# Performance work log

Measured on AMD Instinct MI355X. Metric: run time of the kernel, lower is better.

Reference implementation:

```python
import jax, jax.numpy as jnp
import numpy as np

B, T, N, F_IN, F_OUT = 2, 8, 8192, 128, 32

def setup_inputs() -> dict:
    key = jax.random.key(0)
    k1, k2, k3, k4 = jax.random.split(key, 4)
    inp = jax.random.normal(k1, (B, T, N, F_IN), dtype=jnp.float32)
    adj = jax.random.randint(k2, (N, N), 0, 2, dtype=jnp.int32)
    # xavier_uniform with gain=1.414 ~ std = gain*sqrt(2/(fan_in+fan_out)); gaussian approx
    w_std = 1.414 * np.sqrt(2.0 / (F_IN + F_OUT))
    a_std = 1.414 * np.sqrt(2.0 / (2 * F_OUT + N))
    W = jax.random.normal(k3, (F_IN, F_OUT), dtype=jnp.float32) * w_std
    a = jax.random.normal(k4, (2 * F_OUT, N), dtype=jnp.float32) * a_std
    return {"inp": inp, "adj": adj, "W": W, "a": a}

def reference(inp, adj, W, a):
    # h: [B,T,N,out]
    h = jnp.einsum('btni,io->btno', inp, W)
    out = W.shape[1]
    # mask[j,i] = 1 if j is a neighbor of i (original: torch.where(adj[:, i] > 0))
    mask = (adj > 0).astype(h.dtype)
    # neighbor sum per destination node i: [B,T,N,out]
    nbr = jnp.einsum('ji,btjo->btio', mask, h)
    a1 = a[:out].T   # [N, out], per-node first half of attention vector
    a2 = a[out:].T   # [N, out], per-node second half
    # scalar score per (b,t,i); broadcast across j in the original attention matrix.
    # no-neighbor case coincides since nbr is zero there.
    s = jnp.einsum('btno,no->btn', h, a1) + jnp.einsum('btno,no->btn', nbr, a2)
    # h_prime[b,t,i,:] = s[b,t,i] * sum_j h[b,t,j,:]  (attention row is constant)
    h_prime = s[..., None] * jnp.sum(h, axis=2, keepdims=True)
    return jax.nn.relu(h_prime)
```

## Files before the change

### kernel.cpp

```cpp
#include <hip/hip_runtime.h>

#define BT 16
#define NN 8192
#define FIN 128
#define FOUT 32
#define NB 512
#define SPLITK 4
#define KSPAN (NN / SPLITK)

typedef __attribute__((ext_vector_type(8))) short short8;
typedef __attribute__((ext_vector_type(4))) float float4v;

__device__ __forceinline__ float bf2f(unsigned short u) {
    unsigned v = ((unsigned)u) << 16;
    float f;
    __builtin_memcpy(&f, &v, 4);
    return f;
}
__device__ __forceinline__ unsigned short f2bf(float f) {
    unsigned u;
    __builtin_memcpy(&u, &f, 4);
    u += 0x7FFFu + ((u >> 16) & 1u);
    return (unsigned short)(u >> 16);
}

__global__ void sniff_dtype(const unsigned* __restrict__ Wraw, unsigned* __restrict__ flag,
                            float* __restrict__ sumh) {
    int lane = threadIdx.x;
    unsigned u = Wraw[lane];
    float f = bf2f((unsigned short)(u & 0xFFFFu));
    float af = fabsf(f);
    bool plaus = (af > 1e-5f) && (af < 1e3f);
    unsigned long long msk = __ballot(plaus);
    if (lane == 0) flag[0] = (__popcll(msk) >= 32) ? 1u : 0u;
#pragma unroll
    for (int r = 0; r < 8; ++r) sumh[lane + 64 * r] = 0.f;
}

__launch_bounds__(256)
__global__ void k1(const void* __restrict__ inp_raw, const void* __restrict__ W_raw,
                   unsigned short* __restrict__ Ht, float* __restrict__ sumh,
                   float4* __restrict__ s2v, const unsigned* __restrict__ flagp) {
    __shared__ __align__(16) unsigned short Wt[32 * 136];
    int bid = blockIdx.x;
    const int tid = threadIdx.x;

    if (bid < 128) {
        float4 z; z.x = z.y = z.z = z.w = 0.f;
        s2v[bid * 256 + tid] = z;
        return;
    }
    bid -= 128;
    const int bt = bid >> 6;
    const int j0 = (bid & 63) * 128;
    const bool isbf = (*flagp != 0u);

    if (isbf) {
        const unsigned short* Wb = (const unsigned short*)W_raw;
#pragma unroll
        for (int r = 0; r < 16; ++r) {
            int idx = tid + 256 * r, i = idx >> 5, o = idx & 31;
            Wt[o * 136 + i] = Wb[idx];
        }
    } else {
        const float* Wf = (const float*)W_raw;
#pragma unroll
        for (int r = 0; r < 16; ++r) {
            int idx = tid + 256 * r, i = idx >> 5, o = idx & 31;
            Wt[o * 136 + i] = f2bf(Wf[idx]);
        }
    }
    __syncthreads();

    const int lane = tid & 63, w = tid >> 6;
    const int m = lane & 15, q = lane >> 4;
    const int mt = (w & 1) * 16;
    const int nt = (w >> 1) * 64;

    float4v acc[4];
#pragma unroll
    for (int c = 0; c < 4; ++c) { float4v z = {0.f, 0.f, 0.f, 0.f}; acc[c] = z; }

#pragma unroll
    for (int kstep = 0; kstep < 4; ++kstep) {
        short8 af = *(const short8*)&Wt[(mt + m) * 136 + kstep * 32 + q * 8];
#pragma unroll
        for (int c = 0; c < 4; ++c) {
            int j = j0 + nt + c * 16 + m;
            short8 bfrag;
            if (isbf) {
                bfrag = *(const short8*)((const unsigned short*)inp_raw +
                        ((size_t)bt * NN + j) * FIN + kstep * 32 + q * 8);
            } else {
                const float* fp = (const float*)inp_raw + ((size_t)bt * NN + j) * FIN + kstep * 32 + q * 8;
                float4 f0 = *(const float4*)fp;
                float4 f1 = *(const float4*)(fp + 4);
                union { unsigned short u[8]; short8 v; } t;
                t.u[0] = f2bf(f0.x); t.u[1] = f2bf(f0.y); t.u[2] = f2bf(f0.z); t.u[3] = f2bf(f0.w);
                t.u[4] = f2bf(f1.x); t.u[5] = f2bf(f1.y); t.u[6] = f2bf(f1.z); t.u[7] = f2bf(f1.w);
                bfrag = t.v;
            }
            acc[c] = __builtin_amdgcn_mfma_f32_16x16x32_bf16(af, bfrag, acc[c], 0, 0, 0);
        }
    }

#pragma unroll
    for (int c = 0; c < 4; ++c) {
#pragma unroll
        for (int e = 0; e < 4; ++e) {
            int o = mt + q * 4 + e;
            int j = j0 + nt + c * 16 + m;
            Ht[(size_t)(bt * FOUT + o) * NN + j] = f2bf(acc[c][e]);
        }
    }
#pragma unroll
    for (int e = 0; e < 4; ++e) {
        float s = acc[0][e] + acc[1][e] + acc[2][e] + acc[3][e];
        s += __shfl_xor(s, 1); s += __shfl_xor(s, 2);
        s += __shfl_xor(s, 4); s += __shfl_xor(s, 8);
        if (m == 0) atomicAdd(&sumh[bt * FOUT + mt + q * 4 + e], s);
    }
}

__launch_bounds__(512, 4)
__global__ void k2_fused(const int* __restrict__ adj, const unsigned short* __restrict__ Ht,
                         const void* __restrict__ a_raw, float* __restrict__ s2,
                         const unsigned* __restrict__ flagp) {
    __shared__ int Pl[64 * 65];
    const int tid = threadIdx.x;
    const int lane = tid & 63;
    const int w = tid >> 6;
    const int m = lane & 15, q = lane >> 4;
    const int wn = w * 64;

    const int bid = blockIdx.x;
    const int xcd = bid & 7;
    const int z = xcd >> 1;
    const int ib = (bid >> 3) | ((xcd & 1) << 6);
    const int i0 = ib * 64;
    const int zbase = z * KSPAN;

    {
        const int* arow = adj + (size_t)(zbase + w * 256) * NN + i0 + lane;
#pragma unroll
        for (int u = 0; u < 8; ++u) {
            unsigned wv = 0;
            const int* gp = arow + (size_t)(u * 32) * NN;
#pragma unroll
            for (int j = 0; j < 32; ++j)
                wv |= (__builtin_nontemporal_load(gp + (size_t)j * NN) > 0 ? 1u : 0u) << j;
            Pl[lane * 65 + w * 8 + u] = (int)wv;
        }
    }
    __syncthreads();

    const unsigned short* bp[4];
#pragma unroll
    for (int c = 0; c < 4; ++c)
        bp[c] = Ht + (size_t)(wn + c * 16 + m) * NN + zbase + q * 8;

    float4v acc[4][4];
#pragma unroll
    for (int r = 0; r < 4; ++r)
#pragma unroll
        for (int c = 0; c < 4; ++c) { float4v zz = {0.f, 0.f, 0.f, 0.f}; acc[r][c] = zz; }

#pragma unroll 4
    for (int t = 0; t < 64; ++t) {
        short8 bfr[4];
#pragma unroll
        for (int c = 0; c < 4; ++c)
            bfr[c] = *(const short8*)(bp[c] + t * 32);
        short8 af[4];
#pragma unroll
        for (int r = 0; r < 4; ++r) {
            unsigned word = (unsigned)Pl[(r * 16 + m) * 65 + t];
            unsigned byt = (word >> (q * 8)) & 0xFFu;
            union { unsigned d[4]; short8 v; } tt;
            tt.d[0] = (byt & 1u   ? 0x3F80u : 0u) | (byt & 2u   ? 0x3F800000u : 0u);
            tt.d[1] = (byt & 4u   ? 0x3F80u : 0u) | (byt & 8u   ? 0x3F800000u : 0u);
            tt.d[2] = (byt & 16u  ? 0x3F80u : 0u) | (byt & 32u  ? 0x3F800000u : 0u);
            tt.d[3] = (byt & 64u  ? 0x3F80u : 0u) | (byt & 128u ? 0x3F800000u : 0u);
            af[r] = tt.v;
        }
#pragma unroll
        for (int c = 0; c < 4; ++c)
#pragma unroll
            for (int r = 0; r < 4; ++r)
                acc[r][c] = __builtin_amdgcn_mfma_f32_16x16x32_bf16(af[r], bfr[c], acc[r][c], 0, 0, 0);
    }

    const bool isbf = (*flagp != 0u);
    const int btA = wn >> 5;
#pragma unroll
    for (int r = 0; r < 4; ++r) {
#pragma unroll
        for (int e = 0; e < 4; ++e) {
            int gi = i0 + r * 16 + q * 4 + e;
            float a2m, a2m16;
            if (isbf) {
                const unsigned short* ab = (const unsigned short*)a_raw;
                a2m   = bf2f(ab[(size_t)(FOUT + m) * NN + gi]);
                a2m16 = bf2f(ab[(size_t)(FOUT + 16 + m) * NN + gi]);
            } else {
                const float* afp = (const float*)a_raw;
                a2m   = afp[(size_t)(FOUT + m) * NN + gi];
                a2m16 = afp[(size_t)(FOUT + 16 + m) * NN + gi];
            }
            float sA = acc[r][0][e] * a2m + acc[r][1][e] * a2m16;
            float sB = acc[r][2][e] * a2m + acc[r][3][e] * a2m16;
            sA += __shfl_xor(sA, 1); sA += __shfl_xor(sA, 2);
            sA += __shfl_xor(sA, 4); sA += __shfl_xor(sA, 8);
            sB += __shfl_xor(sB, 1); sB += __shfl_xor(sB, 2);
            sB += __shfl_xor(sB, 4); sB += __shfl_xor(sB, 8);
            if (m == 0) {
                atomicAdd(&s2[(size_t)btA * NN + gi], sA);
                atomicAdd(&s2[(size_t)(btA + 1) * NN + gi], sB);
            }
        }
    }
}

__launch_bounds__(256)
__global__ void k3_out(const unsigned short* __restrict__ Ht, const float* __restrict__ s2,
                       const float* __restrict__ sumh, const void* __restrict__ a_raw,
                       void* __restrict__ out_raw, const unsigned* __restrict__ flagp) {
    const int i = blockIdx.x * 256 + threadIdx.x;
    const int bt = blockIdx.y;
    const bool isbf = (*flagp != 0u);

    float s = s2[(size_t)bt * NN + i];
    if (isbf) {
        const unsigned short* ab = (const unsigned short*)a_raw;
#pragma unroll
        for (int o = 0; o < 32; ++o) {
            float h = bf2f(Ht[(size_t)(bt * FOUT + o) * NN + i]);
            s += h * bf2f(ab[(size_t)o * NN + i]);
        }
    } else {
        const float* afp = (const float*)a_raw;
#pragma unroll
        for (int o = 0; o < 32; ++o) {
            float h = bf2f(Ht[(size_t)(bt * FOUT + o) * NN + i]);
            s += h * afp[(size_t)o * NN + i];
        }
    }

    float ov[32];
#pragma unroll
    for (int o = 0; o < 32; ++o) ov[o] = fmaxf(s * sumh[bt * FOUT + o], 0.f);

    size_t ob = ((size_t)bt * NN + i) * FOUT;
    if (isbf) {
        unsigned short* o16 = (unsigned short*)out_raw + ob;
#pragma unroll
        for (int c = 0; c < 8; ++c) {
            ushort4 p;
            p.x = f2bf(ov[c * 4 + 0]); p.y = f2bf(ov[c * 4 + 1]);
            p.z = f2bf(ov[c * 4 + 2]); p.w = f2bf(ov[c * 4 + 3]);
            *(ushort4*)(o16 + c * 4) = p;
        }
    } else {
        float* of = (float*)out_raw + ob;
#pragma unroll
        for (int c = 0; c < 8; ++c) {
            float4 v;
            v.x = ov[c * 4 + 0]; v.y = ov[c * 4 + 1]; v.z = ov[c * 4 + 2]; v.w = ov[c * 4 + 3];
            *(float4*)(of + c * 4) = v;
        }
    }
}

extern "C" void kernel_launch(void* const* d_in, const int* in_sizes, int n_in,
                              void* d_out, int out_size, void* d_ws, size_t ws_size,
                              hipStream_t stream) {
    const void* inp = d_in[0];
    const int* adj = (const int*)d_in[1];
    const void* W = d_in[2];
    const void* a = d_in[3];

    char* ws = (char*)d_ws;
    unsigned short* Ht = (unsigned short*)ws;
    unsigned* flag = (unsigned*)(ws + 8388608);
    float* s2 = (float*)(ws + 8388608 + 4096);
    float* sumh = (float*)(ws + 8388608 + 4096 + 524288);

    sniff_dtype<<<1, 64, 0, stream>>>((const unsigned*)W, flag, sumh);
    k1<<<1152, 256, 0, stream>>>(inp, W, Ht, sumh, (float4*)s2, flag);
    k2_fused<<<512, 512, 0, stream>>>(adj, Ht, a, s2, flag);
    k3_out<<<dim3(NN / 256, BT), 256, 0, stream>>>(Ht, s2, sumh, a, d_out, flag);
}
```

Before: 557.0 us.

## Move adjacency bit-packing into k1 so it overlaps the H projection

The adjacency mask is now packed into 32-bit bitmasks by 1024 new blocks added to the first kernel, running alongside the projection GEMM blocks, and written to a workspace buffer P. Previously each k2 block read its adjacency slice itself before any MFMA work could start. k2 now reads the packed words straight from global memory inside the MFMA loop, with no shared-memory staging or barrier. In exchange P takes 8 MB of extra workspace and adds a global write and read round trip, and k2 now issues strided global loads in its inner loop.

```diff
diff --git a/kernel.cpp b/kernel.cpp
--- a/kernel.cpp
+++ b/kernel.cpp
@@ -38,9 +38,10 @@
 }
 
 __launch_bounds__(256)
-__global__ void k1(const void* __restrict__ inp_raw, const void* __restrict__ W_raw,
-                   unsigned short* __restrict__ Ht, float* __restrict__ sumh,
-                   float4* __restrict__ s2v, const unsigned* __restrict__ flagp) {
+__global__ void k01(const int* __restrict__ adj, unsigned* __restrict__ P,
+                    const void* __restrict__ inp_raw, const void* __restrict__ W_raw,
+                    unsigned short* __restrict__ Ht, float* __restrict__ sumh,
+                    float4* __restrict__ s2v, const unsigned* __restrict__ flagp) {
     __shared__ __align__(16) unsigned short Wt[32 * 136];
     int bid = blockIdx.x;
     const int tid = threadIdx.x;
@@ -51,6 +52,26 @@
         return;
     }
     bid -= 128;
+    if (bid < 1024) {
+        const int i = (bid & 31) * 256 + tid;
+        const int k0 = (bid >> 5) * 256;
+        const int w0 = k0 >> 5;
+        unsigned words[8];
+#pragma unroll
+        for (int wk = 0; wk < 8; ++wk) {
+            unsigned wv = 0;
+            const int* gp = adj + (size_t)(k0 + wk * 32) * NN + i;
+#pragma unroll
+            for (int kk = 0; kk < 32; ++kk)
+                wv |= (gp[(size_t)kk * NN] > 0 ? 1u : 0u) << kk;
+            words[wk] = wv;
+        }
+#pragma unroll
+        for (int wk = 0; wk < 8; ++wk)
+            P[(size_t)(w0 + wk) * NN + i] = words[wk];
+        return;
+    }
+    bid -= 1024;
     const int bt = bid >> 6;
     const int j0 = (bid & 63) * 128;
     const bool isbf = (*flagp != 0u);
@@ -123,10 +144,9 @@
 }
 
 __launch_bounds__(512, 4)
-__global__ void k2_fused(const int* __restrict__ adj, const unsigned short* __restrict__ Ht,
+__global__ void k2_fused(const unsigned* __restrict__ P, const unsigned short* __restrict__ Ht,
                          const void* __restrict__ a_raw, float* __restrict__ s2,
                          const unsigned* __restrict__ flagp) {
-    __shared__ int Pl[64 * 65];
     const int tid = threadIdx.x;
     const int lane = tid & 63;
     const int w = tid >> 6;
@@ -140,24 +160,14 @@
     const int i0 = ib * 64;
     const int zbase = z * KSPAN;
 
-    {
-        const int* arow = adj + (size_t)(zbase + w * 256) * NN + i0 + lane;
-#pragma unroll
-        for (int u = 0; u < 8; ++u) {
-            unsigned wv = 0;
-            const int* gp = arow + (size_t)(u * 32) * NN;
-#pragma unroll
-            for (int j = 0; j < 32; ++j)
-                wv |= (__builtin_nontemporal_load(gp + (size_t)j * NN) > 0 ? 1u : 0u) << j;
-            Pl[lane * 65 + w * 8 + u] = (int)wv;
-        }
-    }
-    __syncthreads();
-
     const unsigned short* bp[4];
 #pragma unroll
     for (int c = 0; c < 4; ++c)
         bp[c] = Ht + (size_t)(wn + c * 16 + m) * NN + zbase + q * 8;
+    const unsigned* pp[4];
+#pragma unroll
+    for (int r = 0; r < 4; ++r)
+        pp[r] = P + (size_t)(zbase >> 5) * NN + i0 + r * 16 + m;
 
     float4v acc[4][4];
 #pragma unroll
@@ -174,7 +184,7 @@
         short8 af[4];
 #pragma unroll
         for (int r = 0; r < 4; ++r) {
-            unsigned word = (unsigned)Pl[(r * 16 + m) * 65 + t];
+            unsigned word = pp[r][(size_t)t * NN];
             unsigned byt = (word >> (q * 8)) & 0xFFu;
             union { unsigned d[4]; short8 v; } tt;
             tt.d[0] = (byt & 1u   ? 0x3F80u : 0u) | (byt & 2u   ? 0x3F800000u : 0u);
@@ -281,12 +291,13 @@
 
     char* ws = (char*)d_ws;
     unsigned short* Ht = (unsigned short*)ws;
-    unsigned* flag = (unsigned*)(ws + 8388608);
-    float* s2 = (float*)(ws + 8388608 + 4096);
-    float* sumh = (float*)(ws + 8388608 + 4096 + 524288);
+    unsigned* P = (unsigned*)(ws + 8388608);
+    unsigned* flag = (unsigned*)(ws + 16777216);
+    float* s2 = (float*)(ws + 16781312);
+    float* sumh = (float*)(ws + 16781312 + 524288);
 
     sniff_dtype<<<1, 64, 0, stream>>>((const unsigned*)W, flag, sumh);
-    k1<<<1152, 256, 0, stream>>>(inp, W, Ht, sumh, (float4*)s2, flag);
-    k2_fused<<<512, 512, 0, stream>>>(adj, Ht, a, s2, flag);
+    k01<<<2176, 256, 0, stream>>>(adj, P, inp, W, Ht, sumh, (float4*)s2, flag);
+    k2_fused<<<512, 512, 0, stream>>>(P, Ht, a, s2, flag);
     k3_out<<<dim3(NN / 256, BT), 256, 0, stream>>>(Ht, s2, sumh, a, d_out, flag);
 }
```

New measurement: 599.2 us. 7.6% more time.
